# Optimization experiments

Measured on AMD Instinct MI355X. Metric: run time of the kernel, lower is better.

The kernel has to match this reference:

```python
import jax, jax.numpy as jnp
import numpy as np
from jax import lax

DN = ('NCHW', 'OIHW', 'NCHW')

def conv3x3(x, w, b):
    y = lax.conv_general_dilated(x, w, (1, 1), 'SAME', dimension_numbers=DN)
    return y + b[None, :, None, None]

def box_filter(x, ws):
    # depthwise WxW averaging conv, VALID after reflect pad
    C = x.shape[1]
    k = jnp.ones((C, 1, ws, ws), x.dtype) / (ws * ws)
    return lax.conv_general_dilated(x, k, (1, 1), 'VALID', feature_group_count=C,
                                    dimension_numbers=DN)

def compute_std_map(features, ws):
    N, C, H, W = features.shape
    pad = ws // 2
    fp = jnp.pad(features, ((0, 0), (0, 0), (pad, pad), (pad, pad)), mode='reflect')
    local_mean = box_filter(fp, ws)            # [N,C,H,W]
    local_mean_sq = box_filter(fp * fp, ws)
    local_var = jnp.clip(local_mean_sq - local_mean ** 2, 1e-6, None)
    if C == 4:
        cw = jax.nn.softmax(jnp.array([1.0, 1.5, 1.0, 1.5], features.dtype))
    else:
        cw = jax.nn.softmax(jnp.ones((C,), features.dtype))
    result = jnp.sum(jnp.sqrt(local_var) * cw[None, :, None, None], axis=1, keepdims=True)
    return result ** 0.8                        # [N,1,H,W]

def setup_inputs() -> dict:
    key = jax.random.key(0)
    ks = jax.random.split(key, 10)
    inp = {}
    inp['x'] = jax.random.normal(ks[0], (1, 4, 1024, 1024), jnp.float32)
    inp['w1'] = jax.random.normal(ks[1], (32, 4, 3, 3), jnp.float32) * (1.0 / np.sqrt(4 * 9))
    inp['b1'] = jax.random.normal(ks[2], (32,), jnp.float32) * 0.01
    inp['w2'] = jax.random.normal(ks[3], (16, 32, 3, 3), jnp.float32) * (1.0 / np.sqrt(32 * 9))
    inp['b2'] = jax.random.normal(ks[4], (16,), jnp.float32) * 0.01
    inp['w3'] = jax.random.normal(ks[5], (8, 16, 3, 3), jnp.float32) * (1.0 / np.sqrt(16 * 9))
    inp['b3'] = jax.random.normal(ks[6], (8,), jnp.float32) * 0.01
    inp['channel_weights'] = jnp.ones((4,), jnp.float32) / 4.0
    inp['fusion_w'] = jnp.full((1, 3, 1, 1), 1.0 / 3.0, jnp.float32) + \
        jax.random.normal(ks[7], (1, 3, 1, 1), jnp.float32) * 0.02
    inp['fusion_b'] = jnp.zeros((1,), jnp.float32)
    return inp

def reference(x, w1, b1, w2, b2, w3, b3, channel_weights, fusion_w, fusion_b):
    window_sizes = [11, 25, 49]
    # feature extractor
    f = jax.nn.leaky_relu(conv3x3(x, w1, b1), 0.2)
    f = jax.nn.leaky_relu(conv3x3(f, w2, b2), 0.2)
    f = conv3x3(f, w3, b3)                      # [B,8,H,W]
    # multi-scale std maps
    maps = jnp.concatenate([compute_std_map(f, ws) for ws in window_sizes], axis=1)  # [B,3,H,W]
    fused = jax.nn.relu(
        lax.conv_general_dilated(maps, fusion_w, (1, 1), 'VALID', dimension_numbers=DN)
        + fusion_b[None, :, None, None])        # [B,1,H,W]
    # adaptive thresholds
    std_flat = fused.reshape(-1)
    q25 = jnp.quantile(std_flat, 0.25)
    q75 = jnp.quantile(std_flat, 0.75)
    iqr75 = q75 - q25
    global_std = jnp.std(x, axis=(2, 3), keepdims=True, ddof=1)   # [B,4,1,1]
    lower = (q25 - 0.5 * iqr75) * jnp.ones_like(global_std)
    upper = (q75 + 0.5 * iqr75) * jnp.ones_like(global_std)
    gf = jnp.clip(global_std * 5.0, 0.5, 2.0)
    lower = lower * gf
    upper = upper * gf
    cwn = jax.nn.softmax(channel_weights).reshape(1, 4, 1, 1)
    channel_std = jnp.std(x * cwn, axis=(2, 3), keepdims=True, ddof=1)
    cf = jnp.clip(channel_std * 2.0, 0.8, 1.2)
    lower = lower * cf
    upper = upper * cf
    # texture mask
    q30 = jnp.quantile(std_flat, 0.3)
    q70 = jnp.quantile(std_flat, 0.7)
    lower_mean = jnp.mean(lower, axis=1, keepdims=True)           # [B,1,1,1]
    upper_mean = jnp.mean(upper, axis=1, keepdims=True)
    l_t = 0.5 * lower_mean + 0.5 * q30
    u_t = 0.5 * upper_mean + 0.5 * q70
    iqr = q70 - q30
    widen = iqr < 0.01
    l_t = jnp.where(widen, l_t - iqr, l_t)
    u_t = jnp.where(widen, u_t + iqr, u_t)
    diff = u_t - l_t
    mid0 = (l_t + u_t) / 2
    narrow = diff < 0.02
    l_t = jnp.where(narrow, mid0 - 0.01, l_t)
    u_t = jnp.where(narrow, mid0 + 0.01, u_t)
    midpoint = (l_t + u_t) / 2
    scale = u_t - l_t
    normalized = jax.nn.sigmoid(4.0 * (fused - midpoint) / scale)
    nm = jnp.mean(normalized)
    mask = jnp.where(nm > 0.65, 0.1 + 0.5 * normalized,
                     jnp.where(nm < 0.35, 0.2 + 0.5 * normalized,
                               0.15 + 0.55 * normalized))
    return mask
```

## Files before the change

### kernel.cpp

```cpp
#include <hip/hip_runtime.h>
#include <stdint.h>

constexpr int H = 1024, W = 1024;
constexpr int NPIX = H * W;
constexpr int PADM = 24;
constexpr int PROW = W + 2 * PADM;

constexpr size_t OFF_F1H   = 0;
constexpr size_t OFF_F1L   = 67108864;
constexpr size_t OFF_F2H   = 134217728;
constexpr size_t OFF_F2L   = 167772160;
constexpr size_t OFF_F3    = 0;
constexpr size_t OFF_HF    = 33554432;
constexpr size_t OFF_HF2   = 67108864;
constexpr size_t OFF_MAPS  = 100663296;
constexpr size_t OFF_FUSED = OFF_MAPS + 3UL * 4194304;
constexpr size_t OFF_SMALL = 201326592;
constexpr size_t OFF_STATS  = OFF_SMALL;
constexpr size_t OFF_NMSUM  = OFF_SMALL + 64;
constexpr size_t OFF_HIST   = OFF_SMALL + 128;
constexpr size_t OFF_RSTATE = OFF_HIST + 8192;
constexpr size_t OFF_SCAL   = OFF_RSTATE + 64;
constexpr size_t OFF_WT     = OFF_SCAL + 64;

using short8  = __attribute__((ext_vector_type(8))) short;
using short4v = __attribute__((ext_vector_type(4))) short;
using f32x4   = __attribute__((ext_vector_type(4))) float;

__device__ __forceinline__ int reflect1024(int j) {
    return j < 0 ? -j : (j > 1023 ? 2046 - j : j);
}
__device__ __forceinline__ unsigned short rne_bf16(float v) {
    uint32_t u = __float_as_uint(v);
    return (unsigned short)((u + 0x7FFFu + ((u >> 16) & 1u)) >> 16);
}
__device__ __forceinline__ float bf16f(unsigned short h) {
    return __uint_as_float(((uint32_t)h) << 16);
}

__global__ void wfrag_kernel(const float* __restrict__ w, unsigned short* __restrict__ wfH,
                             unsigned short* __restrict__ wfL, int CIN, int COUT, int NF, int S) {
    int total = NF * S * 512;
    int e = blockIdx.x * 256 + threadIdx.x;
    if (e >= total) return;
    int j = e & 7, l = (e >> 3) & 63;
    int rest = e >> 9;
    int s = rest % S, nf = rest / S;
    int k = s * 32 + ((l >> 4) << 3) + j;
    int n = (l & 15) + 16 * nf;
    float v = 0.f;
    if (k < 9 * CIN && n < COUT) {
        int kk = k / CIN, c = k % CIN;
        int ky = kk / 3, kx = kk - ky * 3;
        v = w[((n * CIN + c) * 3 + ky) * 3 + kx];
    }
    unsigned short h = rne_bf16(v);
    wfH[e] = h;
    wfL[e] = rne_bf16(v - bf16f(h));
}

template <int CIN, int COUT, int S, bool LEAKY, int OUT_MODE, int IN_MODE, int MINW>
__global__ __launch_bounds__(256, MINW) void mconv_kernel(
        const void* __restrict__ inA, const void* __restrict__ inB,
        const unsigned short* __restrict__ wfH, const unsigned short* __restrict__ wfL,
        const float* __restrict__ bias, void* __restrict__ outA, void* __restrict__ outB) {
    constexpr int NF = (COUT + 15) / 16;
    constexpr int RS = 66 * CIN;
    __shared__ __align__(16) unsigned short Ah[6 * RS];
    __shared__ __align__(16) unsigned short Al[6 * RS];

    const int tid = threadIdx.x;
    const int bx = blockIdx.x * 64, by = blockIdx.y * 4;
    const int lane = tid & 63, rw = tid >> 6;

    if constexpr (IN_MODE == 1) {
        constexpr int CROW = RS / 8;
        constexpr int LCP  = (CIN == 32) ? 2 : 1;
        constexpr int TOT  = 12 * CROW;
        constexpr int NLOAD = (TOT + 255) / 256;
        const unsigned short* gh = (const unsigned short*)inA;
        const unsigned short* gl = (const unsigned short*)inB;

        short8 regs[NLOAD];
#pragma unroll
        for (int k = 0; k < NLOAD; ++k) {
            int idx = tid + k * 256;
            short8 v = short8{0, 0, 0, 0, 0, 0, 0, 0};
            if (idx < TOT) {
                int ar = idx / CROW;
                int j  = idx - ar * CROW;
                int r  = ar >> 1;
                int a  = ar & 1;
                int gy = by - 1 + r;
                int gx = bx - 1 + (j >> LCP);
                if ((unsigned)gy < 1024u && (unsigned)gx < 1024u) {
                    const unsigned short* g = (a ? gl : gh) +
                        ((size_t)gy << 10) * CIN + (size_t)(bx - 1) * CIN + (size_t)j * 8;
                    v = *(const short8*)g;
                }
            }
            regs[k] = v;
        }
#pragma unroll
        for (int k = 0; k < NLOAD; ++k) {
            int idx = tid + k * 256;
            if (idx < TOT) {
                int ar = idx / CROW;
                int j  = idx - ar * CROW;
                int r  = ar >> 1;
                int a  = ar & 1;
                unsigned short* dst = (a ? Al : Ah) + r * RS + j * 8;
                *(short8*)dst = regs[k];
            }
        }
    } else {
        constexpr int TOT = 6 * 4 * 66;
        constexpr int NLOAD = (TOT + 255) / 256;
        const float* xin = (const float*)inA;
        float regs[NLOAD];
#pragma unroll
        for (int k = 0; k < NLOAD; ++k) {
            int idx = tid + k * 256;
            float v = 0.f;
            if (idx < TOT) {
                int rc  = idx / 66;
                int px  = idx - rc * 66;
                int r   = rc >> 2, c = rc & 3;
                int gy = by - 1 + r, gx = bx - 1 + px;
                if ((unsigned)gy < 1024u && (unsigned)gx < 1024u)
                    v = xin[(size_t)c * NPIX + ((size_t)gy << 10) + gx];
            }
            regs[k] = v;
        }
#pragma unroll
        for (int k = 0; k < NLOAD; ++k) {
            int idx = tid + k * 256;
            if (idx < TOT) {
                int rc  = idx / 66;
                int px  = idx - rc * 66;
                int r   = rc >> 2, c = rc & 3;
                unsigned short h = rne_bf16(regs[k]);
                Ah[r * RS + px * CIN + c] = h;
                Al[r * RS + px * CIN + c] = rne_bf16(regs[k] - bf16f(h));
            }
        }
    }

    short8 wh[NF][S], wl[NF][S];
#pragma unroll
    for (int nf = 0; nf < NF; ++nf)
#pragma unroll
        for (int s = 0; s < S; ++s) {
            wh[nf][s] = *(const short8*)(wfH + (size_t)((nf * S + s) * 64 + lane) * 8);
            wl[nf][s] = *(const short8*)(wfL + (size_t)((nf * S + s) * 64 + lane) * 8);
        }

    const int nidx = lane & 15;
    f32x4 acc[4][NF];
#pragma unroll
    for (int nf = 0; nf < NF; ++nf) {
        float bv = (nidx + nf * 16 < COUT) ? bias[nidx + nf * 16] : 0.f;
#pragma unroll
        for (int t = 0; t < 4; ++t) acc[t][nf] = f32x4{bv, bv, bv, bv};
    }

    __syncthreads();

    if constexpr (CIN == 32) {
        const int base = rw * RS + (lane & 15) * 32 + (lane >> 4) * 8;
        const unsigned short* pah = Ah + base;
        const unsigned short* pal = Al + base;
#pragma unroll
        for (int s = 0; s < S; ++s) {
            const int ky = s / 3, kx = s - (s / 3) * 3;
#pragma unroll
            for (int t = 0; t < 4; ++t) {
                const int off = ky * RS + kx * 32 + t * 512;
                short8 a = *(const short8*)(pah + off);
                short8 b = *(const short8*)(pal + off);
#pragma unroll
                for (int nf = 0; nf < NF; ++nf) {
                    acc[t][nf] = __builtin_amdgcn_mfma_f32_16x16x32_bf16(a, wh[nf][s], acc[t][nf], 0, 0, 0);
                    acc[t][nf] = __builtin_amdgcn_mfma_f32_16x16x32_bf16(b, wh[nf][s], acc[t][nf], 0, 0, 0);
                    acc[t][nf] = __builtin_amdgcn_mfma_f32_16x16x32_bf16(a, wl[nf][s], acc[t][nf], 0, 0, 0);
                }
            }
        }
    } else if constexpr (CIN == 16) {
        const int g23 = lane >> 5;
        const int base = rw * RS + (lane & 15) * 16 + ((lane >> 4) & 1) * 8;
#pragma unroll
        for (int s = 0; s < S; ++s) {
            const int kk0 = 2 * s, kk1 = 2 * s + 1;
            const int O0 = (kk0 / 3) * RS + (kk0 - (kk0 / 3) * 3) * 16;
            const int O1 = (kk1 <= 8) ? (kk1 / 3) * RS + (kk1 - (kk1 / 3) * 3) * 16 : 0;
            const int offs = base + (g23 ? O1 : O0);
#pragma unroll
            for (int t = 0; t < 4; ++t) {
                short8 a = *(const short8*)(Ah + offs + t * 256);
                short8 b = *(const short8*)(Al + offs + t * 256);
#pragma unroll
                for (int nf = 0; nf < NF; ++nf) {
                    acc[t][nf] = __builtin_amdgcn_mfma_f32_16x16x32_bf16(a, wh[nf][s], acc[t][nf], 0, 0, 0);
                    acc[t][nf] = __builtin_amdgcn_mfma_f32_16x16x32_bf16(b, wh[nf][s], acc[t][nf], 0, 0, 0);
                    acc[t][nf] = __builtin_amdgcn_mfma_f32_16x16x32_bf16(a, wl[nf][s], acc[t][nf], 0, 0, 0);
                }
            }
        }
    } else {
        const int base = rw * RS + (lane & 15) * 4;
        const int g2 = (lane >> 4) * 2;
#pragma unroll
        for (int s = 0; s < S; ++s) {
            int kkA = s * 8 + g2, kkB = kkA + 1;
            int kyA = (kkA * 11) >> 5; int kxA = kkA - kyA * 3;
            int poA = (kkA <= 8) ? kyA * RS + kxA * 4 : 0;
            int kyB = (kkB * 11) >> 5; int kxB = kkB - kyB * 3;
            int poB = (kkB <= 8) ? kyB * RS + kxB * 4 : 0;
#pragma unroll
            for (int t = 0; t < 4; ++t) {
                union { short4v q[2]; short8 o; } ua, ub;
                ua.q[0] = *(const short4v*)(Ah + base + poA + t * 64);
                ua.q[1] = *(const short4v*)(Ah + base + poB + t * 64);
                ub.q[0] = *(const short4v*)(Al + base + poA + t * 64);
                ub.q[1] = *(const short4v*)(Al + base + poB + t * 64);
                short8 a = ua.o, b = ub.o;
#pragma unroll
                for (int nf = 0; nf < NF; ++nf) {
                    acc[t][nf] = __builtin_amdgcn_mfma_f32_16x16x32_bf16(a, wh[nf][s], acc[t][nf], 0, 0, 0);
                    acc[t][nf] = __builtin_amdgcn_mfma_f32_16x16x32_bf16(b, wh[nf][s], acc[t][nf], 0, 0, 0);
                    acc[t][nf] = __builtin_amdgcn_mfma_f32_16x16x32_bf16(a, wl[nf][s], acc[t][nf], 0, 0, 0);
                }
            }
        }
    }

    const int y = by + rw;
    const int mrow = (lane >> 4) * 4;
    if constexpr (OUT_MODE == 0) {
        __syncthreads();
        float* smem = (float*)Ah;
        if (nidx < COUT) {
#pragma unroll
            for (int t = 0; t < 4; ++t)
#pragma unroll
                for (int j = 0; j < 4; ++j) {
                    float v = acc[t][0][j];
                    if (LEAKY) v = v >= 0.f ? v : 0.2f * v;
                    smem[(nidx * 4 + rw) * 66 + t * 16 + mrow + j] = v;
                }
        }
        __syncthreads();
        float* outp = (float*)outA;
#pragma unroll
        for (int k = 0; k < (COUT * 256) / 256; ++k) {
            int i = tid + k * 256;
            int px = i & 63, r = (i >> 6) & 3, c = i >> 8;
            outp[(size_t)c * NPIX + ((size_t)(by + r) << 10) + bx + px] =
                smem[(c * 4 + r) * 66 + px];
        }
    } else {
        unsigned short* oh = (unsigned short*)outA;
        unsigned short* ol = (unsigned short*)outB;
#pragma unroll
        for (int t = 0; t < 4; ++t)
#pragma unroll
            for (int nf = 0; nf < NF; ++nf)
#pragma unroll
                for (int j = 0; j < 4; ++j) {
                    float v = acc[t][nf][j];
                    if (LEAKY) v = v >= 0.f ? v : 0.2f * v;
                    int x = bx + t * 16 + mrow + j;
                    size_t off = ((size_t)((y << 10) + x)) * COUT + nf * 16 + nidx;
                    unsigned short hh = rne_bf16(v);
                    oh[off] = hh;
                    ol[off] = rne_bf16(v - bf16f(hh));
                }
    }
}

__global__ void hbox_kernel(const float* __restrict__ f3, float* __restrict__ hf,
                            float* __restrict__ hf2, int p) {
    const int row = blockIdx.x, ch = blockIdx.y, tid = threadIdx.x;
    const float* src = f3 + ch * NPIX + row * W;
    __shared__ float sraw[PROW];
    __shared__ float Pf[PROW + 1], Pf2[PROW + 1];
    __shared__ float wtot[4], wtot2[4];

    for (int i = tid; i < PROW; i += 256)
        sraw[i] = src[reflect1024(i - PADM)];
    __syncthreads();

    float lf[5], lf2[5];
    float sf = 0.f, sf2 = 0.f;
    const int base = tid * 5;
#pragma unroll
    for (int j = 0; j < 5; ++j) {
        int idx = base + j;
        float v = (idx < PROW) ? sraw[idx] : 0.f;
        sf += v;      lf[j] = sf;
        sf2 += v * v; lf2[j] = sf2;
    }
    const int lane = tid & 63, wid = tid >> 6;
    float tf = sf, tf2 = sf2;
#pragma unroll
    for (int off = 1; off < 64; off <<= 1) {
        float a = __shfl_up(tf, off);
        float b = __shfl_up(tf2, off);
        if (lane >= off) { tf += a; tf2 += b; }
    }
    if (lane == 63) { wtot[wid] = tf; wtot2[wid] = tf2; }
    __syncthreads();
    float bse = 0.f, bse2 = 0.f;
    for (int w2 = 0; w2 < wid; ++w2) { bse += wtot[w2]; bse2 += wtot2[w2]; }
    float ex = bse + tf - sf, ex2 = bse2 + tf2 - sf2;
    if (base <= PROW) { Pf[base] = ex; Pf2[base] = ex2; }
#pragma unroll
    for (int j = 0; j < 5; ++j) {
        int idx = base + j + 1;
        if (idx <= PROW) { Pf[idx] = ex + lf[j]; Pf2[idx] = ex2 + lf2[j]; }
    }
    __syncthreads();

    float* df  = hf  + ch * NPIX + row * W;
    float* df2 = hf2 + ch * NPIX + row * W;
    for (int x = tid; x < W; x += 256) {
        int a = x + PADM - p, b = x + PADM + p + 1;
        df[x]  = Pf[b]  - Pf[a];
        df2[x] = Pf2[b] - Pf2[a];
    }
}

constexpr int VRS = 32;
__global__ __launch_bounds__(512) void vbox_kernel(const float* __restrict__ hf,
                                                   const float* __restrict__ hf2,
                                                   float* __restrict__ map,
                                                   int p, float inv_area) {
    const int tid = threadIdx.x;
    const int colIdx = tid & 63, ch = tid >> 6;
    const int col = blockIdx.x * 64 + colIdx;
    const int r0 = blockIdx.y * VRS;
    const float* pf  = hf  + ch * NPIX + col;
    const float* pf2 = hf2 + ch * NPIX + col;

    float S1 = 0.f, S2 = 0.f;
    for (int t = -p; t <= p; ++t) {
        int rr = reflect1024(r0 + t);
        S1 += pf[rr * W];
        S2 += pf2[rr * W];
    }

    __shared__ float ssq[8][8][65];
    const int jj = tid >> 6, cc = tid & 63;
    for (int rb = r0; rb < r0 + VRS; rb += 8) {
#pragma unroll
        for (int j = 0; j < 8; ++j) {
            int r = rb + j;
            float m1 = S1 * inv_area, m2 = S2 * inv_area;
            float var = fmaxf(m2 - m1 * m1, 1e-6f);
            ssq[ch][j][colIdx] = sqrtf(var);
            int radd = reflect1024(r + 1 + p), rsub = reflect1024(r - p);
            S1 += pf[radd * W] - pf[rsub * W];
            S2 += pf2[radd * W] - pf2[rsub * W];
        }
        __syncthreads();
        float a = 0.f;
#pragma unroll
        for (int c8 = 0; c8 < 8; ++c8) a += ssq[c8][jj][cc];
        map[(rb + jj) * W + blockIdx.x * 64 + cc] = powf(a * 0.125f, 0.8f);
        __syncthreads();
    }
}

__global__ void fusion_kernel(const float* __restrict__ maps, const float* __restrict__ fw,
                              const float* __restrict__ fb, float* __restrict__ fused) {
    float w0 = fw[0], w1 = fw[1], w2 = fw[2], b = fb[0];
    for (int i = blockIdx.x * blockDim.x + threadIdx.x; i < NPIX; i += gridDim.x * blockDim.x) {
        float v = maps[i] * w0 + maps[NPIX + i] * w1 + maps[2 * NPIX + i] * w2 + b;
        fused[i] = fmaxf(v, 0.f);
    }
}

__global__ void stats_kernel(const float* __restrict__ x, double* __restrict__ stats) {
    int ch = blockIdx.x >> 6;
    int blk = blockIdx.x & 63;
    const float* p = x + ch * NPIX;
    double s1 = 0.0, s2 = 0.0;
    for (int i = blk * 256 + threadIdx.x; i < NPIX; i += 64 * 256) {
        double v = (double)p[i];
        s1 += v; s2 += v * v;
    }
    __shared__ double b1[256], b2[256];
    b1[threadIdx.x] = s1; b2[threadIdx.x] = s2;
    __syncthreads();
    for (int off = 128; off > 0; off >>= 1) {
        if (threadIdx.x < off) {
            b1[threadIdx.x] += b1[threadIdx.x + off];
            b2[threadIdx.x] += b2[threadIdx.x + off];
        }
        __syncthreads();
    }
    if (threadIdx.x == 0) {
        atomicAdd(&stats[ch * 2 + 0], b1[0]);
        atomicAdd(&stats[ch * 2 + 1], b2[0]);
    }
}

__global__ void init_kernel(double* stats, double* nmsum, uint32_t* hist, uint32_t* rstate) {
    int tid = threadIdx.x;
    for (int i = tid; i < 2048; i += 256) hist[i] = 0u;
    if (tid < 8) stats[tid] = 0.0;
    if (tid == 0) nmsum[0] = 0.0;
    if (tid < 8) rstate[tid] = 0u;
    if (tid < 8) {
        const uint32_t ranks[8] = {262143u, 262144u, 314572u, 314573u,
                                   734002u, 734003u, 786431u, 786432u};
        rstate[8 + tid] = ranks[tid];
    }
}

__global__ void radix_hist_kernel(const float* __restrict__ fused, uint32_t* __restrict__ hist,
                                  const uint32_t* __restrict__ rstate, int pass) {
    __shared__ uint32_t h[8][256];
    int tid = threadIdx.x;
    for (int i = tid; i < 2048; i += 256) ((uint32_t*)h)[i] = 0u;
    __syncthreads();

    uint32_t pref[8];
#pragma unroll
    for (int r = 0; r < 8; ++r) pref[r] = rstate[r];
    uint32_t maskHi = (pass == 0) ? 0u : (0xFFFFFFFFu << (32 - 8 * pass));
    int shift = 24 - 8 * pass;

    for (int i = blockIdx.x * blockDim.x + tid; i < NPIX; i += gridDim.x * blockDim.x) {
        uint32_t u = __float_as_uint(fused[i]);
        uint32_t key = (u & 0x80000000u) ? ~u : (u | 0x80000000u);
        uint32_t bin = (key >> shift) & 0xFFu;
        if (pass == 0) {
            atomicAdd(&h[0][bin], 1u);
        } else {
#pragma unroll
            for (int r = 0; r < 8; ++r) {
                if (((key ^ pref[r]) & maskHi) == 0u)
                    atomicAdd(&h[r][bin], 1u);
            }
        }
    }
    __syncthreads();
    if (pass == 0) {
        for (int i = tid; i < 256; i += 256) {
            uint32_t v = h[0][i];
            if (v)
                for (int r = 0; r < 8; ++r) atomicAdd(&hist[r * 256 + i], v);
        }
    } else {
        for (int i = tid; i < 2048; i += 256) {
            uint32_t v = ((uint32_t*)h)[i];
            if (v) atomicAdd(&hist[i], v);
        }
    }
}

__global__ void radix_scan_kernel(uint32_t* __restrict__ hist, uint32_t* __restrict__ rstate,
                                  int pass) {
    int tid = threadIdx.x;
    int shift = 24 - 8 * pass;
    const int lane = tid & 63, wv = tid >> 6;
    __shared__ uint32_t wsum[4];
    for (int r = 0; r < 8; ++r) {
        uint32_t c = hist[r * 256 + tid];
        uint32_t sc = c;
#pragma unroll
        for (int off = 1; off < 64; off <<= 1) {
            uint32_t t = __shfl_up(sc, off);
            if (lane >= off) sc += t;
        }
        if (lane == 63) wsum[wv] = sc;
        __syncthreads();
        uint32_t base = 0;
        for (int w2 = 0; w2 < wv; ++w2) base += wsum[w2];
        uint32_t incl = base + sc, excl = incl - c;
        uint32_t lr = rstate[8 + r];
        if (lr >= excl && lr < incl) {
            rstate[r] |= ((uint32_t)tid) << shift;
            rstate[8 + r] = lr - excl;
        }
        hist[r * 256 + tid] = 0u;
        __syncthreads();
    }
}

__device__ __forceinline__ float key_to_float(uint32_t k) {
    uint32_t u = (k & 0x80000000u) ? (k & 0x7FFFFFFFu) : ~k;
    return __uint_as_float(u);
}

__global__ void scalar_kernel(const uint32_t* __restrict__ rstate,
                              const double* __restrict__ stats,
                              const float* __restrict__ cw,
                              float* __restrict__ scal) {
    if (threadIdx.x != 0 || blockIdx.x != 0) return;
    float v[8];
#pragma unroll
    for (int r = 0; r < 8; ++r) v[r] = key_to_float(rstate[r]);
    float q25 = v[0] + 0.75f * (v[1] - v[0]);
    float q30 = v[2] + 0.5f * (v[3] - v[2]);
    float q70 = v[4] + 0.5f * (v[5] - v[4]);
    float q75 = v[6] + 0.25f * (v[7] - v[6]);

    const double N = (double)NPIX;
    float gstd[4];
#pragma unroll
    for (int c = 0; c < 4; ++c) {
        double s1 = stats[c * 2 + 0], s2 = stats[c * 2 + 1];
        double var = (s2 - s1 * s1 / N) / (N - 1.0);
        gstd[c] = (float)sqrt(var > 0.0 ? var : 0.0);
    }
    float m = fmaxf(fmaxf(cw[0], cw[1]), fmaxf(cw[2], cw[3]));
    float e0 = expf(cw[0] - m), e1 = expf(cw[1] - m), e2 = expf(cw[2] - m), e3 = expf(cw[3] - m);
    float se = e0 + e1 + e2 + e3;
    float cwn[4] = {e0 / se, e1 / se, e2 / se, e3 / se};

    float iqr75 = q75 - q25;
    float low0 = q25 - 0.5f * iqr75;
    float up0  = q75 + 0.5f * iqr75;
    float lsum = 0.f, usum = 0.f;
#pragma unroll
    for (int c = 0; c < 4; ++c) {
        float gf = fminf(fmaxf(gstd[c] * 5.f, 0.5f), 2.f);
        float cs = cwn[c] * gstd[c];
        float cf = fminf(fmaxf(cs * 2.f, 0.8f), 1.2f);
        lsum += low0 * gf * cf;
        usum += up0 * gf * cf;
    }
    float lmean = 0.25f * lsum, umean = 0.25f * usum;
    float l_t = 0.5f * lmean + 0.5f * q30;
    float u_t = 0.5f * umean + 0.5f * q70;
    float iqr = q70 - q30;
    if (iqr < 0.01f) { l_t -= iqr; u_t += iqr; }
    float diff = u_t - l_t;
    float mid0 = 0.5f * (l_t + u_t);
    if (diff < 0.02f) { l_t = mid0 - 0.01f; u_t = mid0 + 0.01f; }
    scal[0] = 0.5f * (l_t + u_t);
    scal[1] = u_t - l_t;
}

__global__ void sigmoid_kernel(const float* __restrict__ fused, const float* __restrict__ scal,
                               double* __restrict__ nmsum) {
    float mid = scal[0], sc = scal[1];
    float inv = 4.0f / sc;
    float local = 0.f;
    for (int i = blockIdx.x * blockDim.x + threadIdx.x; i < NPIX; i += gridDim.x * blockDim.x) {
        float t = (fused[i] - mid) * inv;
        local += 1.0f / (1.0f + expf(-t));
    }
    __shared__ float red[256];
    red[threadIdx.x] = local;
    __syncthreads();
    for (int off = 128; off > 0; off >>= 1) {
        if (threadIdx.x < off) red[threadIdx.x] += red[threadIdx.x + off];
        __syncthreads();
    }
    if (threadIdx.x == 0) atomicAdd(nmsum, (double)red[0]);
}

__global__ void final_kernel(const float* __restrict__ fused, const float* __restrict__ scal,
                             const double* __restrict__ nmsum, float* __restrict__ out) {
    float nm = (float)(nmsum[0] / (double)NPIX);
    float a, b;
    if (nm > 0.65f)      { a = 0.10f; b = 0.50f; }
    else if (nm < 0.35f) { a = 0.20f; b = 0.50f; }
    else                 { a = 0.15f; b = 0.55f; }
    float mid = scal[0], inv = 4.0f / scal[1];
    for (int i = blockIdx.x * blockDim.x + threadIdx.x; i < NPIX; i += gridDim.x * blockDim.x) {
        float t = (fused[i] - mid) * inv;
        float n = 1.0f / (1.0f + expf(-t));
        out[i] = a + b * n;
    }
}

extern "C" void kernel_launch(void* const* d_in, const int* in_sizes, int n_in,
                              void* d_out, int out_size, void* d_ws, size_t ws_size,
                              hipStream_t stream) {
    const float* x   = (const float*)d_in[0];
    const float* w1  = (const float*)d_in[1];
    const float* b1  = (const float*)d_in[2];
    const float* w2  = (const float*)d_in[3];
    const float* b2  = (const float*)d_in[4];
    const float* w3  = (const float*)d_in[5];
    const float* b3  = (const float*)d_in[6];
    const float* cw  = (const float*)d_in[7];
    const float* fw  = (const float*)d_in[8];
    const float* fb  = (const float*)d_in[9];

    char* ws = (char*)d_ws;
    unsigned short* f1h = (unsigned short*)(ws + OFF_F1H);
    unsigned short* f1l = (unsigned short*)(ws + OFF_F1L);
    unsigned short* f2h = (unsigned short*)(ws + OFF_F2H);
    unsigned short* f2l = (unsigned short*)(ws + OFF_F2L);
    float* f3    = (float*)(ws + OFF_F3);
    float* hf    = (float*)(ws + OFF_HF);
    float* hf2   = (float*)(ws + OFF_HF2);
    float* maps  = (float*)(ws + OFF_MAPS);
    float* fused = (float*)(ws + OFF_FUSED);
    double* stats = (double*)(ws + OFF_STATS);
    double* nmsum = (double*)(ws + OFF_NMSUM);
    uint32_t* hist   = (uint32_t*)(ws + OFF_HIST);
    uint32_t* rstate = (uint32_t*)(ws + OFF_RSTATE);
    float* scal = (float*)(ws + OFF_SCAL);
    unsigned short* wf1H = (unsigned short*)(ws + OFF_WT);
    unsigned short* wf1L = wf1H + 2048;
    unsigned short* wf2H = wf1L + 2048;
    unsigned short* wf2L = wf2H + 4608;
    unsigned short* wf3H = wf2L + 4608;
    unsigned short* wf3L = wf3H + 2560;

    init_kernel<<<1, 256, 0, stream>>>(stats, nmsum, hist, rstate);
    stats_kernel<<<256, 256, 0, stream>>>(x, stats);
    wfrag_kernel<<<(2 * 2 * 512 + 255) / 256, 256, 0, stream>>>(w1, wf1H, wf1L, 4, 32, 2, 2);
    wfrag_kernel<<<(1 * 9 * 512 + 255) / 256, 256, 0, stream>>>(w2, wf2H, wf2L, 32, 16, 1, 9);
    wfrag_kernel<<<(1 * 5 * 512 + 255) / 256, 256, 0, stream>>>(w3, wf3H, wf3L, 16, 8, 1, 5);

    dim3 cgrid(16, 256);
    mconv_kernel<4, 32, 2, true, 1, 0, 4><<<cgrid, 256, 0, stream>>>(
        x, nullptr, wf1H, wf1L, b1, f1h, f1l);
    mconv_kernel<32, 16, 9, true, 1, 1, 3><<<cgrid, 256, 0, stream>>>(
        f1h, f1l, wf2H, wf2L, b2, f2h, f2l);
    mconv_kernel<16, 8, 5, false, 0, 1, 4><<<cgrid, 256, 0, stream>>>(
        f2h, f2l, wf3H, wf3L, b3, f3, nullptr);

    const int wss[3] = {11, 25, 49};
    for (int k = 0; k < 3; ++k) {
        int p = wss[k] / 2;
        float inv_area = 1.0f / (float)(wss[k] * wss[k]);
        hbox_kernel<<<dim3(H, 8), 256, 0, stream>>>(f3, hf, hf2, p);
        vbox_kernel<<<dim3(W / 64, H / VRS), 512, 0, stream>>>(hf, hf2, maps + (size_t)k * NPIX,
                                                               p, inv_area);
    }

    fusion_kernel<<<1024, 256, 0, stream>>>(maps, fw, fb, fused);

    for (int pass = 0; pass < 4; ++pass) {
        radix_hist_kernel<<<256, 256, 0, stream>>>(fused, hist, rstate, pass);
        radix_scan_kernel<<<1, 256, 0, stream>>>(hist, rstate, pass);
    }

    scalar_kernel<<<1, 64, 0, stream>>>(rstate, stats, cw, scal);

    sigmoid_kernel<<<1024, 256, 0, stream>>>(fused, scal, nmsum);
    final_kernel<<<1024, 256, 0, stream>>>(fused, scal, nmsum, (float*)d_out);
}
```

Before: 375.2 us.

## Fuse box filters with fusion, merge prep kernels, truncate bf16 hi split

New measurement: 479.8 us. 27.9% more time.

```diff
diff --git a/kernel.cpp b/kernel.cpp
--- a/kernel.cpp
+++ b/kernel.cpp
@@ -3,22 +3,17 @@
 
 constexpr int H = 1024, W = 1024;
 constexpr int NPIX = H * W;
-constexpr int PADM = 24;
-constexpr int PROW = W + 2 * PADM;
 
 constexpr size_t OFF_F1H   = 0;
 constexpr size_t OFF_F1L   = 67108864;
 constexpr size_t OFF_F2H   = 134217728;
 constexpr size_t OFF_F2L   = 167772160;
 constexpr size_t OFF_F3    = 0;
-constexpr size_t OFF_HF    = 33554432;
-constexpr size_t OFF_HF2   = 67108864;
-constexpr size_t OFF_MAPS  = 100663296;
-constexpr size_t OFF_FUSED = OFF_MAPS + 3UL * 4194304;
-constexpr size_t OFF_SMALL = 201326592;
-constexpr size_t OFF_STATS  = OFF_SMALL;
-constexpr size_t OFF_NMSUM  = OFF_SMALL + 64;
-constexpr size_t OFF_HIST   = OFF_SMALL + 128;
+constexpr size_t OFF_FUSED = 33554432;
+constexpr size_t OFF_SMALL  = 201326592;
+constexpr size_t OFF_PSTAT  = OFF_SMALL;
+constexpr size_t OFF_NMSUM  = OFF_SMALL + 4096;
+constexpr size_t OFF_HIST   = OFF_SMALL + 4160;
 constexpr size_t OFF_RSTATE = OFF_HIST + 8192;
 constexpr size_t OFF_SCAL   = OFF_RSTATE + 64;
 constexpr size_t OFF_WT     = OFF_SCAL + 64;
@@ -38,10 +33,11 @@
     return __uint_as_float(((uint32_t)h) << 16);
 }
 
-__global__ void wfrag_kernel(const float* __restrict__ w, unsigned short* __restrict__ wfH,
-                             unsigned short* __restrict__ wfL, int CIN, int COUT, int NF, int S) {
+__device__ void wfrag_body(const float* __restrict__ w, unsigned short* __restrict__ wfH,
+                           unsigned short* __restrict__ wfL, int CIN, int COUT, int NF, int S,
+                           int blk) {
     int total = NF * S * 512;
-    int e = blockIdx.x * 256 + threadIdx.x;
+    int e = blk * 256 + threadIdx.x;
     if (e >= total) return;
     int j = e & 7, l = (e >> 3) & 63;
     int rest = e >> 9;
@@ -57,6 +53,49 @@
     unsigned short h = rne_bf16(v);
     wfH[e] = h;
     wfL[e] = rne_bf16(v - bf16f(h));
+}
+
+__global__ void prep_kernel(const float* __restrict__ w1, const float* __restrict__ w2,
+                            const float* __restrict__ w3,
+                            unsigned short* wf1H, unsigned short* wf1L,
+                            unsigned short* wf2H, unsigned short* wf2L,
+                            unsigned short* wf3H, unsigned short* wf3L,
+                            const float* __restrict__ x, double* __restrict__ pstats,
+                            double* nmsum, uint32_t* hist, uint32_t* rstate) {
+    __shared__ double sb1[256], sb2[256];
+    const int b = blockIdx.x, tid = threadIdx.x;
+    if (b == 0) {
+        for (int i = tid; i < 2048; i += 256) hist[i] = 0u;
+        if (tid == 0) nmsum[0] = 0.0;
+        if (tid < 8) rstate[tid] = 0u;
+        if (tid < 8) {
+            const uint32_t ranks[8] = {262143u, 262144u, 314572u, 314573u,
+                                       734002u, 734003u, 786431u, 786432u};
+            rstate[8 + tid] = ranks[tid];
+        }
+    } else if (b < 9) {
+        wfrag_body(w1, wf1H, wf1L, 4, 32, 2, 2, b - 1);
+    } else if (b < 27) {
+        wfrag_body(w2, wf2H, wf2L, 32, 16, 1, 9, b - 9);
+    } else if (b < 37) {
+        wfrag_body(w3, wf3H, wf3L, 16, 8, 1, 5, b - 27);
+    } else {
+        int sb = b - 37;
+        int ch = sb >> 6, blk = sb & 63;
+        const float* p = x + (size_t)ch * NPIX;
+        double s1 = 0.0, s2 = 0.0;
+        for (int i = blk * 256 + tid; i < NPIX; i += 64 * 256) {
+            double v = (double)p[i];
+            s1 += v; s2 += v * v;
+        }
+        sb1[tid] = s1; sb2[tid] = s2;
+        __syncthreads();
+        for (int off = 128; off > 0; off >>= 1) {
+            if (tid < off) { sb1[tid] += sb1[tid + off]; sb2[tid] += sb2[tid + off]; }
+            __syncthreads();
+        }
+        if (tid == 0) { pstats[sb * 2] = sb1[0]; pstats[sb * 2 + 1] = sb2[0]; }
+    }
 }
 
 template <int CIN, int COUT, int S, bool LEAKY, int OUT_MODE, int IN_MODE, int MINW>
@@ -139,9 +178,10 @@
                 int rc  = idx / 66;
                 int px  = idx - rc * 66;
                 int r   = rc >> 2, c = rc & 3;
-                unsigned short h = rne_bf16(regs[k]);
-                Ah[r * RS + px * CIN + c] = h;
-                Al[r * RS + px * CIN + c] = rne_bf16(regs[k] - bf16f(h));
+                uint32_t u = __float_as_uint(regs[k]);
+                Ah[r * RS + px * CIN + c] = (unsigned short)(u >> 16);
+                Al[r * RS + px * CIN + c] =
+                    rne_bf16(regs[k] - __uint_as_float(u & 0xFFFF0000u));
             }
         }
     }
@@ -253,7 +293,7 @@
         __syncthreads();
         float* outp = (float*)outA;
 #pragma unroll
-        for (int k = 0; k < (COUT * 256) / 256; ++k) {
+        for (int k = 0; k < COUT; ++k) {
             int i = tid + k * 256;
             int px = i & 63, r = (i >> 6) & 3, c = i >> 8;
             outp[(size_t)c * NPIX + ((size_t)(by + r) << 10) + bx + px] =
@@ -272,150 +312,85 @@
                     if (LEAKY) v = v >= 0.f ? v : 0.2f * v;
                     int x = bx + t * 16 + mrow + j;
                     size_t off = ((size_t)((y << 10) + x)) * COUT + nf * 16 + nidx;
-                    unsigned short hh = rne_bf16(v);
-                    oh[off] = hh;
-                    ol[off] = rne_bf16(v - bf16f(hh));
+                    uint32_t u = __float_as_uint(v);
+                    oh[off] = (unsigned short)(u >> 16);
+                    ol[off] = rne_bf16(v - __uint_as_float(u & 0xFFFF0000u));
                 }
     }
 }
 
-__global__ void hbox_kernel(const float* __restrict__ f3, float* __restrict__ hf,
-                            float* __restrict__ hf2, int p) {
-    const int row = blockIdx.x, ch = blockIdx.y, tid = threadIdx.x;
-    const float* src = f3 + ch * NPIX + row * W;
-    __shared__ float sraw[PROW];
-    __shared__ float Pf[PROW + 1], Pf2[PROW + 1];
-    __shared__ float wtot[4], wtot2[4];
-
-    for (int i = tid; i < PROW; i += 256)
-        sraw[i] = src[reflect1024(i - PADM)];
-    __syncthreads();
-
-    float lf[5], lf2[5];
-    float sf = 0.f, sf2 = 0.f;
-    const int base = tid * 5;
-#pragma unroll
-    for (int j = 0; j < 5; ++j) {
-        int idx = base + j;
-        float v = (idx < PROW) ? sraw[idx] : 0.f;
-        sf += v;      lf[j] = sf;
-        sf2 += v * v; lf2[j] = sf2;
-    }
-    const int lane = tid & 63, wid = tid >> 6;
-    float tf = sf, tf2 = sf2;
-#pragma unroll
-    for (int off = 1; off < 64; off <<= 1) {
-        float a = __shfl_up(tf, off);
-        float b = __shfl_up(tf2, off);
-        if (lane >= off) { tf += a; tf2 += b; }
-    }
-    if (lane == 63) { wtot[wid] = tf; wtot2[wid] = tf2; }
-    __syncthreads();
-    float bse = 0.f, bse2 = 0.f;
-    for (int w2 = 0; w2 < wid; ++w2) { bse += wtot[w2]; bse2 += wtot2[w2]; }
-    float ex = bse + tf - sf, ex2 = bse2 + tf2 - sf2;
-    if (base <= PROW) { Pf[base] = ex; Pf2[base] = ex2; }
-#pragma unroll
-    for (int j = 0; j < 5; ++j) {
-        int idx = base + j + 1;
-        if (idx <= PROW) { Pf[idx] = ex + lf[j]; Pf2[idx] = ex2 + lf2[j]; }
-    }
-    __syncthreads();
-
-    float* df  = hf  + ch * NPIX + row * W;
-    float* df2 = hf2 + ch * NPIX + row * W;
-    for (int x = tid; x < W; x += 256) {
-        int a = x + PADM - p, b = x + PADM + p + 1;
-        df[x]  = Pf[b]  - Pf[a];
-        df2[x] = Pf2[b] - Pf2[a];
-    }
-}
-
-constexpr int VRS = 32;
-__global__ __launch_bounds__(512) void vbox_kernel(const float* __restrict__ hf,
-                                                   const float* __restrict__ hf2,
-                                                   float* __restrict__ map,
-                                                   int p, float inv_area) {
+template <int P>
+__global__ __launch_bounds__(512) void fstd_kernel(const float* __restrict__ f3,
+                                                   const float* __restrict__ fw,
+                                                   const float* __restrict__ fb,
+                                                   float* __restrict__ fused,
+                                                   int kidx, float inv_area) {
+    constexpr int YBS = 32;
+    constexpr int NP = 64 + 2 * P;
     const int tid = threadIdx.x;
-    const int colIdx = tid & 63, ch = tid >> 6;
-    const int col = blockIdx.x * 64 + colIdx;
-    const int r0 = blockIdx.y * VRS;
-    const float* pf  = hf  + ch * NPIX + col;
-    const float* pf2 = hf2 + ch * NPIX + col;
+    const int ch = tid >> 6, lane = tid & 63;
+    const int bx = blockIdx.x * 64;
+    const int r0 = blockIdx.y * YBS;
+
+    __shared__ float P1[8][NP + 2], P2[8][NP + 2];
+    __shared__ float ssq[8][66];
+
+    const float* src = f3 + (size_t)ch * NPIX;
+
+    auto hrow = [&](int rrow, float& h1, float& h2) {
+        const float* rp = src + ((size_t)rrow << 10);
+        float v0 = 0.f, v1 = 0.f;
+        int i0 = 2 * lane;
+        if (i0 < NP) {
+            v0 = rp[reflect1024(bx - P + i0)];
+            if (i0 + 1 < NP) v1 = rp[reflect1024(bx - P + i0 + 1)];
+        }
+        float s  = v0 + v1;
+        float sq = v0 * v0 + v1 * v1;
+        float ts = s, tq = sq;
+#pragma unroll
+        for (int off = 1; off < 64; off <<= 1) {
+            float a = __shfl_up(ts, off);
+            float b = __shfl_up(tq, off);
+            if (lane >= off) { ts += a; tq += b; }
+        }
+        float ex = ts - s, exq = tq - sq;
+        if (i0 <= NP)     { P1[ch][i0] = ex;          P2[ch][i0] = exq; }
+        if (i0 + 1 <= NP) { P1[ch][i0 + 1] = ex + v0; P2[ch][i0 + 1] = exq + v0 * v0; }
+        h1 = P1[ch][lane + 2 * P + 1] - P1[ch][lane];
+        h2 = P2[ch][lane + 2 * P + 1] - P2[ch][lane];
+    };
 
     float S1 = 0.f, S2 = 0.f;
-    for (int t = -p; t <= p; ++t) {
-        int rr = reflect1024(r0 + t);
-        S1 += pf[rr * W];
-        S2 += pf2[rr * W];
-    }
-
-    __shared__ float ssq[8][8][65];
-    const int jj = tid >> 6, cc = tid & 63;
-    for (int rb = r0; rb < r0 + VRS; rb += 8) {
-#pragma unroll
-        for (int j = 0; j < 8; ++j) {
-            int r = rb + j;
-            float m1 = S1 * inv_area, m2 = S2 * inv_area;
-            float var = fmaxf(m2 - m1 * m1, 1e-6f);
-            ssq[ch][j][colIdx] = sqrtf(var);
-            int radd = reflect1024(r + 1 + p), rsub = reflect1024(r - p);
-            S1 += pf[radd * W] - pf[rsub * W];
-            S2 += pf2[radd * W] - pf2[rsub * W];
-        }
-        __syncthreads();
-        float a = 0.f;
-#pragma unroll
-        for (int c8 = 0; c8 < 8; ++c8) a += ssq[c8][jj][cc];
-        map[(rb + jj) * W + blockIdx.x * 64 + cc] = powf(a * 0.125f, 0.8f);
-        __syncthreads();
-    }
-}
-
-__global__ void fusion_kernel(const float* __restrict__ maps, const float* __restrict__ fw,
-                              const float* __restrict__ fb, float* __restrict__ fused) {
-    float w0 = fw[0], w1 = fw[1], w2 = fw[2], b = fb[0];
-    for (int i = blockIdx.x * blockDim.x + threadIdx.x; i < NPIX; i += gridDim.x * blockDim.x) {
-        float v = maps[i] * w0 + maps[NPIX + i] * w1 + maps[2 * NPIX + i] * w2 + b;
-        fused[i] = fmaxf(v, 0.f);
-    }
-}
-
-__global__ void stats_kernel(const float* __restrict__ x, double* __restrict__ stats) {
-    int ch = blockIdx.x >> 6;
-    int blk = blockIdx.x & 63;
-    const float* p = x + ch * NPIX;
-    double s1 = 0.0, s2 = 0.0;
-    for (int i = blk * 256 + threadIdx.x; i < NPIX; i += 64 * 256) {
-        double v = (double)p[i];
-        s1 += v; s2 += v * v;
-    }
-    __shared__ double b1[256], b2[256];
-    b1[threadIdx.x] = s1; b2[threadIdx.x] = s2;
-    __syncthreads();
-    for (int off = 128; off > 0; off >>= 1) {
-        if (threadIdx.x < off) {
-            b1[threadIdx.x] += b1[threadIdx.x + off];
-            b2[threadIdx.x] += b2[threadIdx.x + off];
-        }
-        __syncthreads();
-    }
-    if (threadIdx.x == 0) {
-        atomicAdd(&stats[ch * 2 + 0], b1[0]);
-        atomicAdd(&stats[ch * 2 + 1], b2[0]);
-    }
-}
-
-__global__ void init_kernel(double* stats, double* nmsum, uint32_t* hist, uint32_t* rstate) {
-    int tid = threadIdx.x;
-    for (int i = tid; i < 2048; i += 256) hist[i] = 0u;
-    if (tid < 8) stats[tid] = 0.0;
-    if (tid == 0) nmsum[0] = 0.0;
-    if (tid < 8) rstate[tid] = 0u;
-    if (tid < 8) {
-        const uint32_t ranks[8] = {262143u, 262144u, 314572u, 314573u,
-                                   734002u, 734003u, 786431u, 786432u};
-        rstate[8 + tid] = ranks[tid];
+    for (int t = -P; t <= P; ++t) {
+        float h1, h2;
+        hrow(reflect1024(r0 + t), h1, h2);
+        S1 += h1; S2 += h2;
+    }
+
+    const float w = fw[kidx];
+    const float bias0 = fb[0];
+
+    for (int r = r0; r < r0 + YBS; ++r) {
+        float m1 = S1 * inv_area, m2 = S2 * inv_area;
+        float var = fmaxf(m2 - m1 * m1, 1e-6f);
+        ssq[ch][lane] = sqrtf(var);
+        __syncthreads();
+        if (ch == 0) {
+            float a = 0.f;
+#pragma unroll
+            for (int c = 0; c < 8; ++c) a += ssq[c][lane];
+            float m = powf(a * 0.125f, 0.8f);
+            float* fp = fused + ((size_t)r << 10) + bx + lane;
+            if (kidx == 0)      *fp = bias0 + w * m;
+            else if (kidx == 1) *fp = *fp + w * m;
+            else                *fp = fmaxf(*fp + w * m, 0.f);
+        }
+        float e1, e2, l1, l2;
+        hrow(reflect1024(r + 1 + P), e1, e2);
+        hrow(reflect1024(r - P), l1, l2);
+        S1 += e1 - l1; S2 += e2 - l2;
+        __syncthreads();
     }
 }
 
@@ -461,12 +436,19 @@
     }
 }
 
+__device__ __forceinline__ float key_to_float(uint32_t k) {
+    uint32_t u = (k & 0x80000000u) ? (k & 0x7FFFFFFFu) : ~k;
+    return __uint_as_float(u);
+}
+
 __global__ void radix_scan_kernel(uint32_t* __restrict__ hist, uint32_t* __restrict__ rstate,
-                                  int pass) {
+                                  int pass, const double* __restrict__ pstats,
+                                  const float* __restrict__ cw, float* __restrict__ scal) {
     int tid = threadIdx.x;
     int shift = 24 - 8 * pass;
     const int lane = tid & 63, wv = tid >> 6;
     __shared__ uint32_t wsum[4];
+    __shared__ uint32_t fkey[8];
     for (int r = 0; r < 8; ++r) {
         uint32_t c = hist[r * 256 + tid];
         uint32_t sc = c;
@@ -482,67 +464,72 @@
         uint32_t incl = base + sc, excl = incl - c;
         uint32_t lr = rstate[8 + r];
         if (lr >= excl && lr < incl) {
-            rstate[r] |= ((uint32_t)tid) << shift;
+            uint32_t nk = rstate[r] | (((uint32_t)tid) << shift);
+            rstate[r] = nk;
             rstate[8 + r] = lr - excl;
+            if (pass == 3) fkey[r] = nk;
         }
         hist[r * 256 + tid] = 0u;
         __syncthreads();
     }
-}
-
-__device__ __forceinline__ float key_to_float(uint32_t k) {
-    uint32_t u = (k & 0x80000000u) ? (k & 0x7FFFFFFFu) : ~k;
-    return __uint_as_float(u);
-}
-
-__global__ void scalar_kernel(const uint32_t* __restrict__ rstate,
-                              const double* __restrict__ stats,
-                              const float* __restrict__ cw,
-                              float* __restrict__ scal) {
-    if (threadIdx.x != 0 || blockIdx.x != 0) return;
-    float v[8];
-#pragma unroll
-    for (int r = 0; r < 8; ++r) v[r] = key_to_float(rstate[r]);
-    float q25 = v[0] + 0.75f * (v[1] - v[0]);
-    float q30 = v[2] + 0.5f * (v[3] - v[2]);
-    float q70 = v[4] + 0.5f * (v[5] - v[4]);
-    float q75 = v[6] + 0.25f * (v[7] - v[6]);
-
-    const double N = (double)NPIX;
-    float gstd[4];
-#pragma unroll
-    for (int c = 0; c < 4; ++c) {
-        double s1 = stats[c * 2 + 0], s2 = stats[c * 2 + 1];
-        double var = (s2 - s1 * s1 / N) / (N - 1.0);
-        gstd[c] = (float)sqrt(var > 0.0 ? var : 0.0);
-    }
-    float m = fmaxf(fmaxf(cw[0], cw[1]), fmaxf(cw[2], cw[3]));
-    float e0 = expf(cw[0] - m), e1 = expf(cw[1] - m), e2 = expf(cw[2] - m), e3 = expf(cw[3] - m);
-    float se = e0 + e1 + e2 + e3;
-    float cwn[4] = {e0 / se, e1 / se, e2 / se, e3 / se};
-
-    float iqr75 = q75 - q25;
-    float low0 = q25 - 0.5f * iqr75;
-    float up0  = q75 + 0.5f * iqr75;
-    float lsum = 0.f, usum = 0.f;
-#pragma unroll
-    for (int c = 0; c < 4; ++c) {
-        float gf = fminf(fmaxf(gstd[c] * 5.f, 0.5f), 2.f);
-        float cs = cwn[c] * gstd[c];
-        float cf = fminf(fmaxf(cs * 2.f, 0.8f), 1.2f);
-        lsum += low0 * gf * cf;
-        usum += up0 * gf * cf;
-    }
-    float lmean = 0.25f * lsum, umean = 0.25f * usum;
-    float l_t = 0.5f * lmean + 0.5f * q30;
-    float u_t = 0.5f * umean + 0.5f * q70;
-    float iqr = q70 - q30;
-    if (iqr < 0.01f) { l_t -= iqr; u_t += iqr; }
-    float diff = u_t - l_t;
-    float mid0 = 0.5f * (l_t + u_t);
-    if (diff < 0.02f) { l_t = mid0 - 0.01f; u_t = mid0 + 0.01f; }
-    scal[0] = 0.5f * (l_t + u_t);
-    scal[1] = u_t - l_t;
+
+    if (pass == 3) {
+        double s1 = pstats[2 * tid], s2 = pstats[2 * tid + 1];
+#pragma unroll
+        for (int off = 32; off > 0; off >>= 1) {
+            s1 += __shfl_down(s1, off);
+            s2 += __shfl_down(s2, off);
+        }
+        __shared__ double gs[4][2];
+        if ((tid & 63) == 0) { gs[tid >> 6][0] = s1; gs[tid >> 6][1] = s2; }
+        __syncthreads();
+        if (tid == 0) {
+            float v[8];
+#pragma unroll
+            for (int r = 0; r < 8; ++r) v[r] = key_to_float(fkey[r]);
+            float q25 = v[0] + 0.75f * (v[1] - v[0]);
+            float q30 = v[2] + 0.5f * (v[3] - v[2]);
+            float q70 = v[4] + 0.5f * (v[5] - v[4]);
+            float q75 = v[6] + 0.25f * (v[7] - v[6]);
+
+            const double N = (double)NPIX;
+            float gstd[4];
+#pragma unroll
+            for (int c = 0; c < 4; ++c) {
+                double a1 = gs[c][0], a2 = gs[c][1];
+                double var = (a2 - a1 * a1 / N) / (N - 1.0);
+                gstd[c] = (float)sqrt(var > 0.0 ? var : 0.0);
+            }
+            float m = fmaxf(fmaxf(cw[0], cw[1]), fmaxf(cw[2], cw[3]));
+            float e0 = expf(cw[0] - m), e1 = expf(cw[1] - m);
+            float e2 = expf(cw[2] - m), e3 = expf(cw[3] - m);
+            float se = e0 + e1 + e2 + e3;
+            float cwn[4] = {e0 / se, e1 / se, e2 / se, e3 / se};
+
+            float iqr75 = q75 - q25;
+            float low0 = q25 - 0.5f * iqr75;
+            float up0  = q75 + 0.5f * iqr75;
+            float lsum = 0.f, usum = 0.f;
+#pragma unroll
+            for (int c = 0; c < 4; ++c) {
+                float gf = fminf(fmaxf(gstd[c] * 5.f, 0.5f), 2.f);
+                float cs = cwn[c] * gstd[c];
+                float cf = fminf(fmaxf(cs * 2.f, 0.8f), 1.2f);
+                lsum += low0 * gf * cf;
+                usum += up0 * gf * cf;
+            }
+            float lmean = 0.25f * lsum, umean = 0.25f * usum;
+            float l_t = 0.5f * lmean + 0.5f * q30;
+            float u_t = 0.5f * umean + 0.5f * q70;
+            float iqr = q70 - q30;
+            if (iqr < 0.01f) { l_t -= iqr; u_t += iqr; }
+            float diff = u_t - l_t;
+            float mid0 = 0.5f * (l_t + u_t);
+            if (diff < 0.02f) { l_t = mid0 - 0.01f; u_t = mid0 + 0.01f; }
+            scal[0] = 0.5f * (l_t + u_t);
+            scal[1] = u_t - l_t;
+        }
+    }
 }
 
 __global__ void sigmoid_kernel(const float* __restrict__ fused, const float* __restrict__ scal,
@@ -599,12 +586,9 @@
     unsigned short* f2h = (unsigned short*)(ws + OFF_F2H);
     unsigned short* f2l = (unsigned short*)(ws + OFF_F2L);
     float* f3    = (float*)(ws + OFF_F3);
-    float* hf    = (float*)(ws + OFF_HF);
-    float* hf2   = (float*)(ws + OFF_HF2);
-    float* maps  = (float*)(ws + OFF_MAPS);
     float* fused = (float*)(ws + OFF_FUSED);
-    double* stats = (double*)(ws + OFF_STATS);
-    double* nmsum = (double*)(ws + OFF_NMSUM);
+    double* pstats = (double*)(ws + OFF_PSTAT);
+    double* nmsum  = (double*)(ws + OFF_NMSUM);
     uint32_t* hist   = (uint32_t*)(ws + OFF_HIST);
     uint32_t* rstate = (uint32_t*)(ws + OFF_RSTATE);
     float* scal = (float*)(ws + OFF_SCAL);
@@ -615,11 +599,8 @@
     unsigned short* wf3H = wf2L + 4608;
     unsigned short* wf3L = wf3H + 2560;
 
-    init_kernel<<<1, 256, 0, stream>>>(stats, nmsum, hist, rstate);
-    stats_kernel<<<256, 256, 0, stream>>>(x, stats);
-    wfrag_kernel<<<(2 * 2 * 512 + 255) / 256, 256, 0, stream>>>(w1, wf1H, wf1L, 4, 32, 2, 2);
-    wfrag_kernel<<<(1 * 9 * 512 + 255) / 256, 256, 0, stream>>>(w2, wf2H, wf2L, 32, 16, 1, 9);
-    wfrag_kernel<<<(1 * 5 * 512 + 255) / 256, 256, 0, stream>>>(w3, wf3H, wf3L, 16, 8, 1, 5);
+    prep_kernel<<<293, 256, 0, stream>>>(w1, w2, w3, wf1H, wf1L, wf2H, wf2L, wf3H, wf3L,
+                                         x, pstats, nmsum, hist, rstate);
 
     dim3 cgrid(16, 256);
     mconv_kernel<4, 32, 2, true, 1, 0, 4><<<cgrid, 256, 0, stream>>>(
@@ -629,23 +610,15 @@
     mconv_kernel<16, 8, 5, false, 0, 1, 4><<<cgrid, 256, 0, stream>>>(
         f2h, f2l, wf3H, wf3L, b3, f3, nullptr);
 
-    const int wss[3] = {11, 25, 49};
-    for (int k = 0; k < 3; ++k) {
-        int p = wss[k] / 2;
-        float inv_area = 1.0f / (float)(wss[k] * wss[k]);
-        hbox_kernel<<<dim3(H, 8), 256, 0, stream>>>(f3, hf, hf2, p);
-        vbox_kernel<<<dim3(W / 64, H / VRS), 512, 0, stream>>>(hf, hf2, maps + (size_t)k * NPIX,
-                                                               p, inv_area);
-    }
-
-    fusion_kernel<<<1024, 256, 0, stream>>>(maps, fw, fb, fused);
+    dim3 sgrid(16, 32);
+    fstd_kernel<5><<<sgrid, 512, 0, stream>>>(f3, fw, fb, fused, 0, 1.0f / 121.0f);
+    fstd_kernel<12><<<sgrid, 512, 0, stream>>>(f3, fw, fb, fused, 1, 1.0f / 625.0f);
+    fstd_kernel<24><<<sgrid, 512, 0, stream>>>(f3, fw, fb, fused, 2, 1.0f / 2401.0f);
 
     for (int pass = 0; pass < 4; ++pass) {
         radix_hist_kernel<<<256, 256, 0, stream>>>(fused, hist, rstate, pass);
-        radix_scan_kernel<<<1, 256, 0, stream>>>(hist, rstate, pass);
-    }
-
-    scalar_kernel<<<1, 64, 0, stream>>>(rstate, stats, cw, scal);
+        radix_scan_kernel<<<1, 256, 0, stream>>>(hist, rstate, pass, pstats, cw, scal);
+    }
 
     sigmoid_kernel<<<1024, 256, 0, stream>>>(fused, scal, nmsum);
     final_kernel<<<1024, 256, 0, stream>>>(fused, scal, nmsum, (float*)d_out);
```
